# Kernel tuning notes

Measured on AMD Instinct MI355X. Metric: run time of the kernel, lower is better.

Reference implementation:

```python
import jax, jax.numpy as jnp
import numpy as np
import math

NUM_HEADS = 4
NUM_GROUPS = 32  # model_channel
EPS = 1e-5

def setup_inputs() -> dict:
    key = jax.random.key(0)
    ks = jax.random.split(key, 4)
    B, C, H, W, D = 2, 256, 16, 16, 16
    x = jax.random.normal(ks[0], (B, C, H, W, D), dtype=jnp.float32)
    norm_w = jnp.ones((C,), jnp.float32)
    norm_b = jnp.zeros((C,), jnp.float32)
    qkv_w = jax.random.normal(ks[1], (3 * C, C), jnp.float32) * (1.0 / math.sqrt(C))
    proj_w = jax.random.normal(ks[2], (C, C), jnp.float32) * (1.0 / math.sqrt(C))
    proj_b = jnp.zeros((C,), jnp.float32)
    return {"x": x, "norm_w": norm_w, "norm_b": norm_b, "qkv_w": qkv_w,
            "proj_w": proj_w, "proj_b": proj_b}

def reference(x, norm_w, norm_b, qkv_w, proj_w, proj_b):
    B, C, H, W, D = x.shape
    T = H * W * D
    xf = x.reshape(B, C, T)
    # GroupNorm over (C//G, T) per group
    G = NUM_GROUPS
    xg = xf.reshape(B, G, C // G, T)
    mean = xg.mean(axis=(2, 3), keepdims=True)
    var = xg.var(axis=(2, 3), keepdims=True)
    xn = ((xg - mean) * jax.lax.rsqrt(var + EPS)).reshape(B, C, T)
    xn = xn * norm_w[None, :, None] + norm_b[None, :, None]
    # qkv 1x1x1 conv (no bias): [B, 3C, T]
    qkv = jnp.einsum('oc,bct->bot', qkv_w, xn)
    h = NUM_HEADS
    qkv = qkv.reshape(B * h, 3 * C // h, T)
    q, k, v = jnp.split(qkv, 3, axis=1)  # each [B*h, C//h, T]
    scale = 1.0 / math.sqrt(math.sqrt(C // h))
    attn = jnp.einsum('bct,bcs->bts', q * scale, k * scale)  # [B*h, T, T]
    attn = jax.nn.softmax(attn, axis=-1)
    out = jnp.einsum('bts,bcs->bct', attn, v).reshape(B, C, T)
    out = jnp.einsum('oc,bct->bot', proj_w, out) + proj_b[None, :, None]
    return (xf + out).reshape(B, C, H, W, D)
```

## Files before the change

### kernel.cpp

```cpp
#include <hip/hip_runtime.h>
#include <hip/hip_bf16.h>

typedef __hip_bfloat16 bf16;
typedef __bf16 bf16x8 __attribute__((ext_vector_type(8)));
typedef float f32x2 __attribute__((ext_vector_type(2)));
typedef float f32x4 __attribute__((ext_vector_type(4)));
typedef float f32x16 __attribute__((ext_vector_type(16)));

#define MFMA16(a,b,c) __builtin_amdgcn_mfma_f32_16x16x32_bf16(a,b,c,0,0,0)
#define MFMA32(a,b,c) __builtin_amdgcn_mfma_f32_32x32x16_bf16(a,b,c,0,0,0)

static __device__ __forceinline__ bf16x8 ld8(const bf16* p){
  return *reinterpret_cast<const bf16x8*>(p);
}
static __device__ __forceinline__ unsigned pk(float a, float b){
  __hip_bfloat162 h = __float22bfloat162_rn(make_float2(a, b));
  return *reinterpret_cast<unsigned*>(&h);
}

#define GLL(src, dst) __builtin_amdgcn_global_load_lds( \
    (const __attribute__((address_space(1))) unsigned int*)(src), \
    (__attribute__((address_space(3))) unsigned int*)(dst), 16, 0, 0)

__global__ void k_wgs1(const float* __restrict__ qw, const float* __restrict__ pw,
                       bf16* __restrict__ qwb, bf16* __restrict__ pwb,
                       const float* __restrict__ x, float* __restrict__ gpart){
  int bx = blockIdx.x;
  int tid = threadIdx.x;
  if (bx < 768){
    int i = bx*256 + tid;
    int o = i >> 8;
    int j = o % 192;
    float f = (j < 64) ? 0.51006973f
            : (j < 128) ? 0.35355339f : 1.0f;
    qwb[i] = __float2bfloat16(qw[i]*f);
    if (i < 256*256) pwb[i] = __float2bfloat16(pw[i]);
    return;
  }
  int idx = bx - 768;
  int glin = idx >> 3;
  int s = idx & 7;
  const float* xb = x + (size_t)glin*8*4096 + s*512;
  const float* p = xb + (size_t)(tid>>5)*4096 + (tid&31)*16;
  float s1 = 0.f, s2 = 0.f;
  #pragma unroll
  for (int i = 0; i < 4; i++){
    float4 v = *(const float4*)(p + i*4);
    s1 += (v.x+v.y)+(v.z+v.w);
    s2 += (v.x*v.x+v.y*v.y)+(v.z*v.z+v.w*v.w);
  }
  #pragma unroll
  for (int d = 1; d < 64; d <<= 1){ s1 += __shfl_xor(s1,d); s2 += __shfl_xor(s2,d); }
  __shared__ float r1[4], r2[4];
  int w = tid >> 6;
  if ((tid & 63) == 0){ r1[w] = s1; r2[w] = s2; }
  __syncthreads();
  if (tid == 0){
    gpart[(glin*8+s)*2+0] = (r1[0]+r1[1])+(r1[2]+r1[3]);
    gpart[(glin*8+s)*2+1] = (r2[0]+r2[1])+(r2[2]+r2[3]);
  }
}

__global__ __launch_bounds__(512,2) void k_gqkv(const float* __restrict__ x,
      const float* __restrict__ gpart, const float* __restrict__ nw,
      const float* __restrict__ nb, const bf16* __restrict__ wb,
      bf16* __restrict__ q, bf16* __restrict__ k, bf16* __restrict__ v){
  int t0 = blockIdx.x * 32;
  int b  = blockIdx.y;
  int tid = threadIdx.x;
  __shared__ bf16 tcm[256][36];
  __shared__ bf16 tlB[32][264];
  __shared__ float2 scb[256];

  if (tid < 256){
    int c = tid;
    int glin = b*32 + (c>>3);
    float s1=0.f, s2=0.f;
    #pragma unroll
    for (int s=0;s<8;s++){ s1+=gpart[(glin*8+s)*2]; s2+=gpart[(glin*8+s)*2+1]; }
    float mean = s1*(1.f/32768.f);
    float var = s2*(1.f/32768.f)-mean*mean;
    float rstd = rsqrtf(var+1e-5f);
    float sc = nw[c]*rstd;
    scb[c] = make_float2(sc, nb[c]-mean*sc);
  }
  __syncthreads();
  {
    int c = tid>>1, half = tid&1;
    float2 sb = scb[c];
    const float* xr = x + ((size_t)(b*256+c))*4096 + t0 + half*16;
    #pragma unroll
    for (int j=0;j<4;j++){
      float4 vv = *(const float4*)(xr + j*4);
      uint2 uu;
      uu.x = pk(vv.x*sb.x+sb.y, vv.y*sb.x+sb.y);
      uu.y = pk(vv.z*sb.x+sb.y, vv.w*sb.x+sb.y);
      *(uint2*)&tcm[c][half*16 + j*4] = uu;
    }
  }
  __syncthreads();
  #pragma unroll
  for (int pass=0; pass<2; ++pass){
    int idx = tid + pass*512;
    int t = idx >> 5, c8 = idx & 31;
    unsigned short us[8];
    #pragma unroll
    for (int j=0;j<8;j++) us[j] = *(unsigned short*)&tcm[c8*8+j][t];
    uint4 o;
    o.x = us[0]|((unsigned)us[1]<<16); o.y = us[2]|((unsigned)us[3]<<16);
    o.z = us[4]|((unsigned)us[5]<<16); o.w = us[6]|((unsigned)us[7]<<16);
    *(uint4*)&tlB[t][c8*8] = o;
  }
  __syncthreads();

  int w = tid>>6, L = tid&63, l15 = L&15, lg = L>>4;
  f32x4 acc[6][2] = {};
  const bf16* arow = wb + (size_t)(w*96 + l15)*256 + lg*8;
  #pragma unroll
  for (int kk=0;kk<8;kk++){
    bf16x8 bbf[2];
    #pragma unroll
    for (int n=0;n<2;n++) bbf[n] = ld8(&tlB[n*16+l15][kk*32 + lg*8]);
    #pragma unroll
    for (int ot=0;ot<6;ot++){
      bf16x8 a = ld8(arow + (size_t)ot*16*256 + kk*32);
      #pragma unroll
      for (int n=0;n<2;n++) acc[ot][n] = MFMA16(a, bbf[n], acc[ot][n]);
    }
  }
  #pragma unroll
  for (int ot=0;ot<6;ot++){
    #pragma unroll
    for (int n=0;n<2;n++){
      int t = t0 + n*16 + l15;
      #pragma unroll
      for (int i=0;i<4;i++){
        int o = w*96 + ot*16 + lg*4 + i;
        int hh = o/192, j = o%192;
        int bh = b*4 + hh;
        float val = acc[ot][n][i];
        if (j<64)        q[((size_t)bh*4096+t)*64+j] = __float2bfloat16(val);
        else if (j<128)  k[((size_t)bh*4096+t)*64+(j-64)] = __float2bfloat16(val);
        else             v[((size_t)bh*64+(j-128))*4096+t] = __float2bfloat16(val);
      }
    }
  }
}

__global__ __launch_bounds__(512,2) void k_attn(const bf16* __restrict__ q,
      const char* __restrict__ kg_, const char* __restrict__ vg_,
      char* __restrict__ opart, float* __restrict__ lsumP, int ssplit){
  const int bh = blockIdx.x;
  const int qg = blockIdx.y * 256;
  const int z  = blockIdx.z;
  const int slen = 4096 / ssplit;
  const int niters = slen >> 6;
  const int s_begin = z * slen;
  const int tid = threadIdx.x;
  const int w = tid >> 6, L = tid & 63, l31 = L & 31, hi = L >> 5;

  __shared__ __align__(16) char kb[3][8192];
  __shared__ __align__(16) char vb[3][8192];

  bf16x8 qf[4];
  {
    const bf16* qr = q + (size_t)bh*4096*64 + (size_t)(qg + w*32 + l31)*64 + hi*8;
    #pragma unroll
    for (int ch = 0; ch < 4; ch++)
      qf[ch] = ld8(qr + ch*16);
  }

  const char* kg = kg_ + ((size_t)bh<<19);
  const char* vg = vg_ + ((size_t)bh<<19);
  const int row = w*8 + (L>>3);
  const int sx  = (((L&7) ^ (L>>3)) << 4);

  #define STAGE(buf, t) do { \
    int ss = s_begin + (t)*64; \
    GLL(kg + (size_t)(ss + row)*128 + sx, (char*)&kb[buf][0] + w*1024); \
    GLL(vg + (size_t)row*8192 + ss*2 + sx, (char*)&vb[buf][0] + w*1024); \
  } while(0)

  STAGE(0, 0);
  STAGE(1, 1);
  f32x16 oaccT[2] = {};
  f32x2 lsum2 = {0.f, 0.f};
  const int kxor = (l31 & 7) << 4;
  const float NSH = -11.5415603f;
  int cur = 0, n2 = 2;

  for (int t = 0; t < niters; ++t){
    if (t < niters-1) asm volatile("s_waitcnt vmcnt(2)" ::: "memory");
    else              asm volatile("s_waitcnt vmcnt(0)" ::: "memory");
    __builtin_amdgcn_s_barrier();
    if (t + 2 < niters) STAGE(n2, t+2);

    const char* kc = &kb[cur][0];
    const char* vc = &vb[cur][0];
    #pragma unroll
    for (int sc2 = 0; sc2 < 2; ++sc2){
      bf16x8 kf[4];
      int srow = sc2*32 + l31;
      #pragma unroll
      for (int ch = 0; ch < 4; ++ch)
        kf[ch] = *(const bf16x8*)(kc + srow*128 + ((ch*32 + hi*16) ^ kxor));
      f32x16 sacc;
      #pragma unroll
      for (int r = 0; r < 16; ++r) sacc[r] = NSH;
      __builtin_amdgcn_s_setprio(1);
      #pragma unroll
      for (int ch = 0; ch < 4; ++ch)
        sacc = MFMA32(kf[ch], qf[ch], sacc);
      __builtin_amdgcn_s_setprio(0);
      #pragma unroll
      for (int sc = 0; sc < 2; ++sc){
        float p0 = __builtin_amdgcn_exp2f(sacc[sc*8+0]);
        float p1 = __builtin_amdgcn_exp2f(sacc[sc*8+1]);
        float p2 = __builtin_amdgcn_exp2f(sacc[sc*8+2]);
        float p3 = __builtin_amdgcn_exp2f(sacc[sc*8+3]);
        float p4 = __builtin_amdgcn_exp2f(sacc[sc*8+4]);
        float p5 = __builtin_amdgcn_exp2f(sacc[sc*8+5]);
        float p6 = __builtin_amdgcn_exp2f(sacc[sc*8+6]);
        float p7 = __builtin_amdgcn_exp2f(sacc[sc*8+7]);
        f32x2 e0 = {p0, p1}, e1 = {p2, p3}, e2 = {p4, p5}, e3 = {p6, p7};
        lsum2 += (e0 + e1) + (e2 + e3);
        unsigned pa0 = pk(p0, p1);
        unsigned pa1 = pk(p2, p3);
        unsigned pb0 = pk(p4, p5);
        unsigned pb1 = pk(p6, p7);
        asm("v_permlane32_swap_b32 %0, %1" : "+v"(pa0), "+v"(pb0));
        asm("v_permlane32_swap_b32 %0, %1" : "+v"(pa1), "+v"(pb1));
        union { unsigned u[4]; bf16x8 v; } pu;
        pu.u[0]=pa0; pu.u[1]=pa1; pu.u[2]=pb0; pu.u[3]=pb1;
        bf16x8 vfa = *(const bf16x8*)(vc + (l31)*128      + ((sc2*64 + sc*32 + hi*16) ^ kxor));
        bf16x8 vfb = *(const bf16x8*)(vc + (32+l31)*128   + ((sc2*64 + sc*32 + hi*16) ^ kxor));
        __builtin_amdgcn_s_setprio(1);
        oaccT[0] = MFMA32(vfa, pu.v, oaccT[0]);
        oaccT[1] = MFMA32(vfb, pu.v, oaccT[1]);
        __builtin_amdgcn_s_setprio(0);
      }
    }
    cur = (cur==2)?0:cur+1;
    n2  = (n2==2)?0:n2+1;
  }
  #undef STAGE

  char* ob = opart + (size_t)(bh*ssplit + z)*4096*128;
  {
    float ls = lsum2[0] + lsum2[1];
    ls += __shfl_xor(ls, 32);
    int qrow = qg + w*32 + l31;
    if (hi == 0) lsumP[(size_t)(bh*ssplit+z)*4096 + qrow] = ls;
    #pragma unroll
    for (int ct = 0; ct < 2; ++ct)
      #pragma unroll
      for (int b2 = 0; b2 < 4; ++b2){
        unsigned w0 = pk(oaccT[ct][b2*4+0], oaccT[ct][b2*4+1]);
        unsigned w1 = pk(oaccT[ct][b2*4+2], oaccT[ct][b2*4+3]);
        uint2 val; val.x = w0; val.y = w1;
        *(uint2*)(ob + (size_t)qrow*128 + (ct*32 + b2*8 + hi*4)*2) = val;
      }
  }
}

__global__ void k_oproj(const char* __restrict__ opart, const float* __restrict__ lsumP,
                        const bf16* __restrict__ pwb, const float* __restrict__ pb,
                        const float* __restrict__ x, float* __restrict__ out, int ssplit){
  int t0 = blockIdx.x * 32;
  int b  = blockIdx.y;
  int tid = threadIdx.x;
  __shared__ bf16 tl[32][280];

  {
    int rrow = tid >> 3;
    int cs = (tid & 7) * 8;
    #pragma unroll
    for (int h = 0; h < 4; ++h){
      int bh = b*4 + h;
      int qrow = t0 + rrow;
      float l = 0.f, o[8] = {};
      for (int z = 0; z < ssplit; ++z){
        size_t base = (size_t)(bh*ssplit + z)*4096 + qrow;
        l += lsumP[base];
        uint4 u = *(const uint4*)(opart + base*128 + cs*2);
        unsigned uu[4] = {u.x, u.y, u.z, u.w};
        #pragma unroll
        for (int j = 0; j < 4; ++j){
          unsigned lobits = (uu[j] & 0xffffu) << 16;
          unsigned hibits = uu[j] & 0xffff0000u;
          o[2*j]   += *reinterpret_cast<float*>(&lobits);
          o[2*j+1] += *reinterpret_cast<float*>(&hibits);
        }
      }
      float inv = 1.f / l;
      uint4 wv;
      wv.x = pk(o[0]*inv, o[1]*inv); wv.y = pk(o[2]*inv, o[3]*inv);
      wv.z = pk(o[4]*inv, o[5]*inv); wv.w = pk(o[6]*inv, o[7]*inv);
      *(uint4*)&tl[rrow][h*64 + cs] = wv;
    }
  }
  __syncthreads();

  int w = tid >> 6, L = tid & 63, l15 = L & 15, lg = L >> 4;
  f32x4 acc[4][2] = {};
  const bf16* arow = pwb + (size_t)(w*64 + l15)*256 + lg*8;
  #pragma unroll
  for (int kk = 0; kk < 8; kk++){
    bf16x8 a[4];
    #pragma unroll
    for (int i = 0; i < 4; i++) a[i] = ld8(arow + i*16*256 + kk*32);
    bf16x8 bb[2];
    #pragma unroll
    for (int n = 0; n < 2; n++) bb[n] = ld8(&tl[n*16 + l15][kk*32 + lg*8]);
    #pragma unroll
    for (int i = 0; i < 4; i++)
      #pragma unroll
      for (int n = 0; n < 2; n++)
        acc[i][n] = MFMA16(a[i], bb[n], acc[i][n]);
  }
  #pragma unroll
  for (int i = 0; i < 4; i++){
    #pragma unroll
    for (int ii = 0; ii < 4; ii++){
      int o = w*64 + i*16 + lg*4 + ii;
      float bias = pb[o];
      const float* xr = x + ((size_t)(b*256 + o))*4096 + t0;
      float* orow = out + ((size_t)(b*256 + o))*4096 + t0;
      #pragma unroll
      for (int n = 0; n < 2; n++){
        int tt = n*16 + l15;
        orow[tt] = acc[i][n][ii] + bias + xr[tt];
      }
    }
  }
}

extern "C" void kernel_launch(void* const* d_in, const int* in_sizes, int n_in,
                              void* d_out, int out_size, void* d_ws, size_t ws_size,
                              hipStream_t stream){
  const float* x     = (const float*)d_in[0];
  const float* nw    = (const float*)d_in[1];
  const float* nb    = (const float*)d_in[2];
  const float* qkvw  = (const float*)d_in[3];
  const float* projw = (const float*)d_in[4];
  const float* projb = (const float*)d_in[5];
  float* out = (float*)d_out;
  char* ws = (char*)d_ws;
  bf16* qwb   = (bf16*)(ws);
  bf16* pwb   = (bf16*)(ws + 393216);
  bf16* q     = (bf16*)(ws + 524288);
  char* kk    = (ws + 524288 + 4194304);
  char* v     = (ws + 524288 + 2*4194304);
  size_t off_opart = 524288 + (size_t)3*4194304;
  size_t need8 = off_opart + (size_t)8*8*4096*128 + (size_t)8*8*4096*4 + 8192;
  int ssplit = (ws_size >= need8) ? 8 : 4;
  char*  opart = ws + off_opart;
  size_t off_lsum  = off_opart + (size_t)8*ssplit*4096*128;
  float* lsum  = (float*)(ws + off_lsum);
  size_t off_gpart = off_lsum + (size_t)8*ssplit*4096*4;
  float* gpart = (float*)(ws + off_gpart);

  k_wgs1<<<1280, 256, 0, stream>>>(qkvw, projw, qwb, pwb, x, gpart);
  k_gqkv<<<dim3(128,2), 512, 0, stream>>>(x, gpart, nw, nb, qwb, q, (bf16*)kk, (bf16*)v);
  k_attn<<<dim3(8,16,ssplit), 512, 0, stream>>>(q, kk, v, opart, lsum, ssplit);
  k_oproj<<<dim3(128,2), 256, 0, stream>>>(opart, lsum, pwb, projb, x, out, ssplit);
}
```

Before: 100.6 us.

## Load K/V tiles directly from global into registers instead of LDS staging

The attention kernel drops the triple-buffered global_load_lds staging of K and V, along with its barriers. Each wave now loads its K and V fragments straight from global memory into registers. The block shrinks from 512 to 256 threads with 128 query rows, and the grid doubles in y to cover the same work. This removes LDS traffic and block-wide synchronisation, but K/V tiles are no longer shared across waves, so global/L2 reads multiply and load latency is exposed without explicit prefetching.

Measured after the change: 175.5 us. 74.5% more time.

```diff
diff --git a/kernel.cpp b/kernel.cpp
--- a/kernel.cpp
+++ b/kernel.cpp
@@ -17,10 +17,6 @@
   __hip_bfloat162 h = __float22bfloat162_rn(make_float2(a, b));
   return *reinterpret_cast<unsigned*>(&h);
 }
-
-#define GLL(src, dst) __builtin_amdgcn_global_load_lds( \
-    (const __attribute__((address_space(1))) unsigned int*)(src), \
-    (__attribute__((address_space(3))) unsigned int*)(dst), 16, 0, 0)
 
 __global__ void k_wgs1(const float* __restrict__ qw, const float* __restrict__ pw,
                        bf16* __restrict__ qwb, bf16* __restrict__ pwb,
@@ -147,11 +143,11 @@
   }
 }
 
-__global__ __launch_bounds__(512,2) void k_attn(const bf16* __restrict__ q,
+__global__ __launch_bounds__(256,2) void k_attn(const bf16* __restrict__ q,
       const char* __restrict__ kg_, const char* __restrict__ vg_,
       char* __restrict__ opart, float* __restrict__ lsumP, int ssplit){
   const int bh = blockIdx.x;
-  const int qg = blockIdx.y * 256;
+  const int qg = blockIdx.y * 128;
   const int z  = blockIdx.z;
   const int slen = 4096 / ssplit;
   const int niters = slen >> 6;
@@ -159,9 +155,6 @@
   const int tid = threadIdx.x;
   const int w = tid >> 6, L = tid & 63, l31 = L & 31, hi = L >> 5;
 
-  __shared__ __align__(16) char kb[3][8192];
-  __shared__ __align__(16) char vb[3][8192];
-
   bf16x8 qf[4];
   {
     const bf16* qr = q + (size_t)bh*4096*64 + (size_t)(qg + w*32 + l31)*64 + hi*8;
@@ -170,40 +163,30 @@
       qf[ch] = ld8(qr + ch*16);
   }
 
-  const char* kg = kg_ + ((size_t)bh<<19);
-  const char* vg = vg_ + ((size_t)bh<<19);
-  const int row = w*8 + (L>>3);
-  const int sx  = (((L&7) ^ (L>>3)) << 4);
-
-  #define STAGE(buf, t) do { \
-    int ss = s_begin + (t)*64; \
-    GLL(kg + (size_t)(ss + row)*128 + sx, (char*)&kb[buf][0] + w*1024); \
-    GLL(vg + (size_t)row*8192 + ss*2 + sx, (char*)&vb[buf][0] + w*1024); \
-  } while(0)
-
-  STAGE(0, 0);
-  STAGE(1, 1);
+  const char* krow = kg_ + ((size_t)bh<<19) + (size_t)l31*128 + hi*16;
+  const char* vrow = vg_ + ((size_t)bh<<19) + (size_t)l31*8192 + hi*16;
+
   f32x16 oaccT[2] = {};
   f32x2 lsum2 = {0.f, 0.f};
-  const int kxor = (l31 & 7) << 4;
   const float NSH = -11.5415603f;
-  int cur = 0, n2 = 2;
-
+
+  #pragma unroll 2
   for (int t = 0; t < niters; ++t){
-    if (t < niters-1) asm volatile("s_waitcnt vmcnt(2)" ::: "memory");
-    else              asm volatile("s_waitcnt vmcnt(0)" ::: "memory");
-    __builtin_amdgcn_s_barrier();
-    if (t + 2 < niters) STAGE(n2, t+2);
-
-    const char* kc = &kb[cur][0];
-    const char* vc = &vb[cur][0];
+    int s0 = s_begin + t*64;
     #pragma unroll
     for (int sc2 = 0; sc2 < 2; ++sc2){
+      const char* kb = krow + (size_t)(s0 + sc2*32)*128;
       bf16x8 kf[4];
-      int srow = sc2*32 + l31;
       #pragma unroll
       for (int ch = 0; ch < 4; ++ch)
-        kf[ch] = *(const bf16x8*)(kc + srow*128 + ((ch*32 + hi*16) ^ kxor));
+        kf[ch] = ld8((const bf16*)(kb + ch*32));
+      bf16x8 vf[2][2];
+      #pragma unroll
+      for (int sc = 0; sc < 2; ++sc){
+        const char* vb = vrow + (size_t)(s0*2) + sc2*64 + sc*32;
+        vf[sc][0] = ld8((const bf16*)(vb));
+        vf[sc][1] = ld8((const bf16*)(vb + (size_t)32*8192));
+      }
       f32x16 sacc;
       #pragma unroll
       for (int r = 0; r < 16; ++r) sacc[r] = NSH;
@@ -232,18 +215,13 @@
         asm("v_permlane32_swap_b32 %0, %1" : "+v"(pa1), "+v"(pb1));
         union { unsigned u[4]; bf16x8 v; } pu;
         pu.u[0]=pa0; pu.u[1]=pa1; pu.u[2]=pb0; pu.u[3]=pb1;
-        bf16x8 vfa = *(const bf16x8*)(vc + (l31)*128      + ((sc2*64 + sc*32 + hi*16) ^ kxor));
-        bf16x8 vfb = *(const bf16x8*)(vc + (32+l31)*128   + ((sc2*64 + sc*32 + hi*16) ^ kxor));
         __builtin_amdgcn_s_setprio(1);
-        oaccT[0] = MFMA32(vfa, pu.v, oaccT[0]);
-        oaccT[1] = MFMA32(vfb, pu.v, oaccT[1]);
+        oaccT[0] = MFMA32(vf[sc][0], pu.v, oaccT[0]);
+        oaccT[1] = MFMA32(vf[sc][1], pu.v, oaccT[1]);
         __builtin_amdgcn_s_setprio(0);
       }
     }
-    cur = (cur==2)?0:cur+1;
-    n2  = (n2==2)?0:n2+1;
-  }
-  #undef STAGE
+  }
 
   char* ob = opart + (size_t)(bh*ssplit + z)*4096*128;
   {
@@ -362,6 +340,6 @@
 
   k_wgs1<<<1280, 256, 0, stream>>>(qkvw, projw, qwb, pwb, x, gpart);
   k_gqkv<<<dim3(128,2), 512, 0, stream>>>(x, gpart, nw, nb, qwb, q, (bf16*)kk, (bf16*)v);
-  k_attn<<<dim3(8,16,ssplit), 512, 0, stream>>>(q, kk, v, opart, lsum, ssplit);
+  k_attn<<<dim3(8,32,ssplit), 256, 0, stream>>>(q, kk, v, opart, lsum, ssplit);
   k_oproj<<<dim3(128,2), 256, 0, stream>>>(opart, lsum, pwb, projb, x, out, ssplit);
 }
```

## Store K and V in MFMA-fragment-packed layout for contiguous LDS reads

Applied to the files above, without the earlier changes.

The QKV projection kernel now writes K and V in a pre-tiled layout that matches the MFMA operand fragments: each 1 KB block holds one 32-row by 16-byte-per-lane fragment. The attention kernel then stages each block with one contiguous global-to-LDS load per wave and reads fragments at lane*16 offsets, with no XOR swizzle. This removes per-thread address arithmetic and the swizzle, and makes global loads fully contiguous. The cost is scattered, non-coalesced bf16 stores in the projection kernel, and the correctness of the new indexing has to be kept consistent between producer and consumer.

Result: no change. 98.94 us (-1.6%).

```diff
diff --git a/kernel.cpp b/kernel.cpp
--- a/kernel.cpp
+++ b/kernel.cpp
@@ -138,10 +138,18 @@
         int o = w*96 + ot*16 + lg*4 + i;
         int hh = o/192, j = o%192;
         int bh = b*4 + hh;
-        float val = acc[ot][n][i];
-        if (j<64)        q[((size_t)bh*4096+t)*64+j] = __float2bfloat16(val);
-        else if (j<128)  k[((size_t)bh*4096+t)*64+(j-64)] = __float2bfloat16(val);
-        else             v[((size_t)bh*64+(j-128))*4096+t] = __float2bfloat16(val);
+        bf16 val = __float2bfloat16(acc[ot][n][i]);
+        if (j<64){
+          q[((size_t)bh*4096+t)*64+j] = val;
+        } else if (j<128){
+          int kc = j-64;
+          k[((size_t)((bh*128 + (t>>5))*4 + (kc>>4)))*512
+            + ((t&31) + ((kc>>3)&1)*32)*8 + (kc&7)] = val;
+        } else {
+          int vc = j-128;
+          v[((size_t)((bh*256 + (t>>4))*2 + (vc>>5)))*512
+            + ((vc&31) + ((t>>3)&1)*32)*8 + (t&7)] = val;
+        }
       }
     }
   }
@@ -172,20 +180,17 @@
 
   const char* kg = kg_ + ((size_t)bh<<19);
   const char* vg = vg_ + ((size_t)bh<<19);
-  const int row = w*8 + (L>>3);
-  const int sx  = (((L&7) ^ (L>>3)) << 4);
 
   #define STAGE(buf, t) do { \
     int ss = s_begin + (t)*64; \
-    GLL(kg + (size_t)(ss + row)*128 + sx, (char*)&kb[buf][0] + w*1024); \
-    GLL(vg + (size_t)row*8192 + ss*2 + sx, (char*)&vb[buf][0] + w*1024); \
+    GLL(kg + (size_t)((ss>>5) + (w>>2))*4096 + (w&3)*1024 + L*16, (char*)&kb[buf][0] + w*1024); \
+    GLL(vg + (size_t)((ss>>4) + (w>>1))*2048 + (w&1)*1024 + L*16, (char*)&vb[buf][0] + w*1024); \
   } while(0)
 
   STAGE(0, 0);
   STAGE(1, 1);
   f32x16 oaccT[2] = {};
   f32x2 lsum2 = {0.f, 0.f};
-  const int kxor = (l31 & 7) << 4;
   const float NSH = -11.5415603f;
   int cur = 0, n2 = 2;
 
@@ -200,10 +205,9 @@
     #pragma unroll
     for (int sc2 = 0; sc2 < 2; ++sc2){
       bf16x8 kf[4];
-      int srow = sc2*32 + l31;
       #pragma unroll
       for (int ch = 0; ch < 4; ++ch)
-        kf[ch] = *(const bf16x8*)(kc + srow*128 + ((ch*32 + hi*16) ^ kxor));
+        kf[ch] = *(const bf16x8*)(kc + (sc2*4 + ch)*1024 + L*16);
       f32x16 sacc;
       #pragma unroll
       for (int r = 0; r < 16; ++r) sacc[r] = NSH;
@@ -232,8 +236,8 @@
         asm("v_permlane32_swap_b32 %0, %1" : "+v"(pa1), "+v"(pb1));
         union { unsigned u[4]; bf16x8 v; } pu;
         pu.u[0]=pa0; pu.u[1]=pa1; pu.u[2]=pb0; pu.u[3]=pb1;
-        bf16x8 vfa = *(const bf16x8*)(vc + (l31)*128      + ((sc2*64 + sc*32 + hi*16) ^ kxor));
-        bf16x8 vfb = *(const bf16x8*)(vc + (32+l31)*128   + ((sc2*64 + sc*32 + hi*16) ^ kxor));
+        bf16x8 vfa = *(const bf16x8*)(vc + ((sc2*2+sc)*2 + 0)*1024 + L*16);
+        bf16x8 vfb = *(const bf16x8*)(vc + ((sc2*2+sc)*2 + 1)*1024 + L*16);
         __builtin_amdgcn_s_setprio(1);
         oaccT[0] = MFMA32(vfa, pu.v, oaccT[0]);
         oaccT[1] = MFMA32(vfb, pu.v, oaccT[1]);
```
